# Optimization experiments

Hardware: AMD Instinct MI355X
Metric: run time of the kernel (lower is better)

## Reference

```python
import jax, jax.numpy as jnp
import numpy as np

B, T, C, H = 4, 4096, 1024, 128

def setup_inputs() -> dict:
    key = jax.random.key(0)
    kx, kq, kk, kv = jax.random.split(key, 4)
    s = 1.0 / np.sqrt(C)  # linear-layer-like init scale
    return {
        "x": jax.random.normal(kx, (B, T, C), dtype=jnp.float32),
        "Wq": jax.random.normal(kq, (C, H), dtype=jnp.float32) * s,
        "Wk": jax.random.normal(kk, (C, H), dtype=jnp.float32) * s,
        "Wv": jax.random.normal(kv, (C, H), dtype=jnp.float32) * s,
    }

def reference(x, Wq, Wk, Wv):
    # q,k,v: [B,T,H]
    q = jnp.einsum('btc,ch->bth', x, Wq)
    k = jnp.einsum('btc,ch->bth', x, Wk)
    v = jnp.einsum('btc,ch->bth', x, Wv)
    # scores: [B,T,T]  (NOTE: source applies no 1/sqrt(H) scaling)
    wei = jnp.einsum('bth,bih->bti', q, k)
    t = x.shape[1]
    causal = jnp.tril(jnp.ones((t, t), dtype=bool))
    wei = jnp.where(causal, wei, -jnp.inf)
    probs = jax.nn.softmax(wei, axis=-1)
    out = jnp.einsum('btj,bjh->bth', probs, v)
    return out
```

## Files before the change

### kernel.cpp

```cpp
#include <hip/hip_runtime.h>

#define B_ 4
#define T_ 4096
#define C_ 1024
#define H_ 128

typedef __attribute__((ext_vector_type(8))) __bf16 bf16x8;
typedef __attribute__((ext_vector_type(8))) unsigned short u16x8;
typedef __attribute__((ext_vector_type(4))) float f32x4;
typedef __attribute__((ext_vector_type(4))) unsigned int u32x4;

__device__ __forceinline__ unsigned short f2bf(float f) {
  unsigned int u = __float_as_uint(f);
  return (unsigned short)((u + 0x7FFFu + ((u >> 16) & 1u)) >> 16);
}
__device__ __forceinline__ float bf2f(unsigned short h) {
  return __uint_as_float((unsigned)h << 16);
}
__device__ __forceinline__ bf16x8 ldb8(const unsigned short* p) {
  return *(const bf16x8*)(const void*)p;
}
__device__ __forceinline__ void async16(void* lds, const void* g) {
  __builtin_amdgcn_global_load_lds(
      (const __attribute__((address_space(1))) unsigned int*)g,
      (__attribute__((address_space(3))) unsigned int*)lds, 16, 0, 0);
}
__device__ __forceinline__ void split8a(const float* f, bf16x8& hi, bf16x8& lo) {
  u16x8 h, l;
#pragma unroll
  for (int j = 0; j < 8; j++) {
    h[j] = f2bf(f[j]);
    l[j] = f2bf(f[j] - bf2f(h[j]));
  }
  hi = __builtin_bit_cast(bf16x8, h);
  lo = __builtin_bit_cast(bf16x8, l);
}


__global__ void wt_k(const float* __restrict__ Wq, const float* __restrict__ Wk,
                     const float* __restrict__ Wv, unsigned short* __restrict__ Whi,
                     unsigned short* __restrict__ Wlo) {
  __shared__ float tile[32][33];
  int m = blockIdx.z;
  const float* W = (m == 0) ? Wq : ((m == 1) ? Wk : Wv);
  int c0 = blockIdx.x * 32, h0 = blockIdx.y * 32;
  int tx = threadIdx.x, ty = threadIdx.y;
#pragma unroll
  for (int i = 0; i < 4; i++)
    tile[ty + 8 * i][tx] = W[(size_t)(c0 + ty + 8 * i) * H_ + h0 + tx];
  __syncthreads();
  size_t base = (size_t)m * H_ * C_;
#pragma unroll
  for (int i = 0; i < 4; i++) {
    float f = tile[tx][ty + 8 * i];
    unsigned short hi = f2bf(f);
    int h = h0 + ty + 8 * i;
    int kg = c0 + tx;
    int w0 = kg >> 6, c = (kg >> 3) & 7, e = kg & 7;
    size_t idx = base + (size_t)h * C_ + w0 * 64 + ((c + (h & 7)) & 7) * 8 + e;
    Whi[idx] = hi;
    if (m < 2) Wlo[idx] = f2bf(f - bf2f(hi));
  }
}

__global__ __launch_bounds__(256, 3) void qkv_k(
    const float* __restrict__ x, const unsigned short* __restrict__ Whi,
    const unsigned short* __restrict__ Wlo, unsigned short* __restrict__ Qhi,
    unsigned short* __restrict__ Qlo, unsigned short* __restrict__ Khf,
    unsigned short* __restrict__ Klf, unsigned short* __restrict__ Vf) {
  int m = blockIdx.x % 3;
  int r0 = (blockIdx.x / 3) * 64;
  __shared__ __align__(16) float sx[64 * 64];
  __shared__ __align__(16) unsigned short swh[128 * 64];
  __shared__ __align__(16) unsigned short swl[128 * 64];
  int tid = threadIdx.x;
  int lane = tid & 63, wave = tid >> 6;
  int l15 = lane & 15, quad = lane >> 4;
  const unsigned short* Wmh = Whi + (size_t)m * H_ * C_;
  const unsigned short* Wml = Wlo + (size_t)m * H_ * C_;
  f32x4 acc[8];
#pragma unroll
  for (int n = 0; n < 8; n++) acc[n] = (f32x4){0.f, 0.f, 0.f, 0.f};

  for (int k0 = 0; k0 < C_; k0 += 64) {
    __syncthreads();
#pragma unroll
    for (int i = 0; i < 4; i++) {
      int s = (wave * 4 + i) * 64 + lane;
      {
        int tr = s >> 4, p = s & 15;
        async16((unsigned short*)sx + (size_t)(wave * 4 + i) * 512,
                x + (size_t)(r0 + tr) * C_ + k0 + ((p - tr) & 15) * 4);
      }
      {
        int hr = s >> 3, p = s & 7;
        async16(swh + (size_t)(wave * 4 + i) * 512,
                Wmh + (size_t)hr * C_ + k0 + p * 8);
        if (m < 2)
          async16(swl + (size_t)(wave * 4 + i) * 512,
                  Wml + (size_t)hr * C_ + k0 + p * 8);
      }
    }
    __syncthreads();
#pragma unroll
    for (int kk = 0; kk < 2; kk++) {
      float xa[8];
#pragma unroll
      for (int half = 0; half < 2; half++) {
        int p = (kk * 8 + quad * 2 + half + l15) & 15;
        *(f32x4*)&xa[half * 4] =
            *(const f32x4*)(const void*)(sx + (wave * 16 + l15) * 64 + p * 4);
      }
      bf16x8 ahi, alo;
      split8a(xa, ahi, alo);
      if (m < 2) {
#pragma unroll
        for (int n = 0; n < 8; n++) {
          int p = (kk * 4 + quad + l15) & 7;
          bf16x8 bhi = ldb8(swh + (n * 16 + l15) * 64 + p * 8);
          bf16x8 blo = ldb8(swl + (n * 16 + l15) * 64 + p * 8);
          acc[n] = __builtin_amdgcn_mfma_f32_16x16x32_bf16(ahi, bhi, acc[n], 0, 0, 0);
          acc[n] = __builtin_amdgcn_mfma_f32_16x16x32_bf16(alo, bhi, acc[n], 0, 0, 0);
          acc[n] = __builtin_amdgcn_mfma_f32_16x16x32_bf16(ahi, blo, acc[n], 0, 0, 0);
        }
      } else {
#pragma unroll
        for (int n = 0; n < 8; n++) {
          int p = (kk * 4 + quad + l15) & 7;
          bf16x8 bhi = ldb8(swh + (n * 16 + l15) * 64 + p * 8);
          acc[n] = __builtin_amdgcn_mfma_f32_16x16x32_bf16(ahi, bhi, acc[n], 0, 0, 0);
        }
      }
    }
  }
  int ob = r0 + wave * 16 + quad * 4;
  if (m == 0) {
#pragma unroll
    for (int n8 = 0; n8 < 8; n8++)
#pragma unroll
      for (int r = 0; r < 4; r++) {
        float f = acc[n8][r];
        unsigned short hi = f2bf(f);
        size_t idx = (size_t)(ob + r) * H_ + n8 * 16 + l15;
        Qhi[idx] = hi;
        Qlo[idx] = f2bf(f - bf2f(hi));
      }
  } else if (m == 1) {
#pragma unroll
    for (int n8 = 0; n8 < 8; n8++)
#pragma unroll
      for (int r = 0; r < 4; r++) {
        int gr = ob + r;
        int bb = gr >> 12, t = gr & (T_ - 1);
        int kt = t >> 6, tr = t & 63, nf = tr >> 4, lk = tr & 15;
        int h = n8 * 16 + l15;
        int kkf = h >> 5, qk = (h >> 3) & 3, e = h & 7;
        size_t idx = (size_t)bb * T_ * H_ +
                     (size_t)((kt * 16 + nf * 4 + kkf) * 64 + qk * 16 + lk) * 8 + e;
        float f = acc[n8][r];
        unsigned short hi = f2bf(f);
        Khf[idx] = hi;
        Klf[idx] = f2bf(f - bf2f(hi));
      }
  } else {
#pragma unroll
    for (int n8 = 0; n8 < 8; n8++)
#pragma unroll
      for (int r = 0; r < 4; r++) {
        int gr = ob + r;
        int bb = gr >> 12, t = gr & (T_ - 1);
        int kt = t >> 6, ks = (t >> 5) & 1, qv = (t >> 3) & 3, jj = t & 7;
        size_t idx = (size_t)bb * T_ * H_ +
                     (size_t)((kt * 16 + ks * 8 + n8) * 64 + qv * 16 + l15) * 8 + jj;
        Vf[idx] = f2bf(acc[n8][r]);
      }
  }
}

__device__ __forceinline__ bf16x8 sm_tile(f32x4* s, float& mr, float& lr,
                                          f32x4* o, int lane) {
  int l15 = lane & 15, quad = lane >> 4;
  float mx = fmaxf(fmaxf(fmaxf(s[0][0], s[0][1]), fmaxf(s[0][2], s[0][3])),
                   fmaxf(fmaxf(s[1][0], s[1][1]), fmaxf(s[1][2], s[1][3])));
  mx = fmaxf(mx, __shfl_xor(mx, 16));
  mx = fmaxf(mx, __shfl_xor(mx, 32));
  float mi = fmaxf(mr, mx);
  float al = __expf(mr - mi);
  mr = mi;
#pragma unroll
  for (int n16 = 0; n16 < 2; n16++)
#pragma unroll
    for (int r = 0; r < 4; r++) s[n16][r] = __expf(s[n16][r] - mi);
  float sum = ((s[0][0] + s[0][1]) + (s[0][2] + s[0][3])) +
              ((s[1][0] + s[1][1]) + (s[1][2] + s[1][3]));
  sum += __shfl_xor(sum, 16);
  sum += __shfl_xor(sum, 32);
  lr = lr * al + sum;
  float alo[4];
#pragma unroll
  for (int r = 0; r < 4; r++) alo[r] = __shfl(al, quad * 4 + r);
#pragma unroll
  for (int nv = 0; nv < 8; nv++)
#pragma unroll
    for (int r = 0; r < 4; r++) o[nv][r] *= alo[r];
  unsigned W[2][2];
#pragma unroll
  for (int n16 = 0; n16 < 2; n16++)
#pragma unroll
    for (int j = 0; j < 2; j++)
      W[n16][j] = (unsigned)f2bf(s[n16][2 * j]) |
                  ((unsigned)f2bf(s[n16][2 * j + 1]) << 16);
  int base = ((lane >> 4) & 1) * 32 + l15;
  unsigned A[4];
#pragma unroll
  for (int a = 0; a < 4; a++) {
    int src = base + (a >> 1) * 16;
    unsigned lo = (unsigned)__shfl((int)W[0][a & 1], src);
    unsigned hi = (unsigned)__shfl((int)W[1][a & 1], src);
    A[a] = (lane & 32) ? hi : lo;
  }
  u32x4 aw = (u32x4){A[0], A[1], A[2], A[3]};
  return __builtin_bit_cast(bf16x8, aw);
}

__global__ __launch_bounds__(256, 2) void flash4_k(
    const unsigned short* __restrict__ Qhi, const unsigned short* __restrict__ Qlo,
    const unsigned short* __restrict__ Khf, const unsigned short* __restrict__ Klf,
    const unsigned short* __restrict__ Vf, float* __restrict__ opart,
    float2* __restrict__ mlpart) {
  __shared__ __align__(16) unsigned short skh[2][4096];
  __shared__ __align__(16) unsigned short skl[2][4096];
  __shared__ __align__(16) unsigned short sv[2][4096];
  int tid = threadIdx.x;
  int wave = tid >> 6, lane = tid & 63;
  int l15 = lane & 15, quad = lane >> 4;

  int n = blockIdx.x;
  int h = n >> 4;
  int p = (h < 16) ? (31 - h) : (h - 16);
  int g = n & 15;
  int sp = g >> 2, b = g & 3;
  int q0 = p << 7;
  int ktB = sp * (p + 1);
  int nt = p + 1;
  size_t boff = (size_t)b * T_ * H_;
  const unsigned short* Khb = Khf + boff;
  const unsigned short* Klb = Klf + boff;
  const unsigned short* Vb = Vf + boff;

  bf16x8 qh0[4], ql0[4], qh1[4], ql1[4];
  {
    const unsigned short* qrh =
        Qhi + boff + (size_t)(q0 + wave * 32 + l15) * H_ + quad * 8;
    const unsigned short* qrl =
        Qlo + boff + (size_t)(q0 + wave * 32 + l15) * H_ + quad * 8;
#pragma unroll
    for (int kk = 0; kk < 4; kk++) {
      qh0[kk] = ldb8(qrh + kk * 32);
      ql0[kk] = ldb8(qrl + kk * 32);
      qh1[kk] = ldb8(qrh + 16 * H_ + kk * 32);
      ql1[kk] = ldb8(qrl + 16 * H_ + kk * 32);
    }
  }
  f32x4 o0[8], o1[8];
#pragma unroll
  for (int nn = 0; nn < 8; nn++) {
    o0[nn] = (f32x4){0.f, 0.f, 0.f, 0.f};
    o1[nn] = (f32x4){0.f, 0.f, 0.f, 0.f};
  }
  float mr0 = -1e30f, mr1 = -1e30f, lr0 = 0.f, lr1 = 0.f;

  int rmin = q0 + wave * 32;
  int ch = wave * 2;

#define STAGE(kt32_, d_)                                                        \
  {                                                                             \
    size_t gbase = (size_t)(kt32_)*4096 + (size_t)ch * 512 + (size_t)lane * 8;  \
    async16(&skh[d_][ch * 512], Khb + gbase);                                   \
    async16(&skh[d_][(ch + 1) * 512], Khb + gbase + 512);                       \
    async16(&skl[d_][ch * 512], Klb + gbase);                                   \
    async16(&skl[d_][(ch + 1) * 512], Klb + gbase + 512);                       \
    async16(&sv[d_][ch * 512], Vb + gbase);                                     \
    async16(&sv[d_][(ch + 1) * 512], Vb + gbase + 512);                         \
  }

  STAGE(ktB, 0);
  int cur = 0;
  for (int it = 0; it < nt; ++it) {
    int kt32 = ktB + it;
    if (it + 1 < nt) {
      STAGE(kt32 + 1, cur ^ 1);
      asm volatile("s_waitcnt vmcnt(6)" ::: "memory");
    } else {
      asm volatile("s_waitcnt vmcnt(0)" ::: "memory");
    }
    __builtin_amdgcn_s_barrier();
    int c0k = kt32 << 5;
    bool t1a = (c0k <= rmin + 31);
    bool t0a = (c0k <= rmin + 15);
    if (t1a) {
      f32x4 s0[2], s1[2];
#pragma unroll
      for (int n16 = 0; n16 < 2; ++n16) {
        s0[n16] = (f32x4){0.f, 0.f, 0.f, 0.f};
        s1[n16] = (f32x4){0.f, 0.f, 0.f, 0.f};
      }
      __builtin_amdgcn_s_setprio(1);
#pragma unroll
      for (int n16 = 0; n16 < 2; ++n16) {
        bf16x8 kh[4], kl[4];
#pragma unroll
        for (int kk = 0; kk < 4; kk++) {
          kh[kk] = ldb8(&skh[cur][(n16 * 4 + kk) * 512 + lane * 8]);
          kl[kk] = ldb8(&skl[cur][(n16 * 4 + kk) * 512 + lane * 8]);
        }
#pragma unroll
        for (int kk = 0; kk < 4; kk++) {
          s1[n16] = __builtin_amdgcn_mfma_f32_16x16x32_bf16(kh[kk], qh1[kk], s1[n16], 0, 0, 0);
          s1[n16] = __builtin_amdgcn_mfma_f32_16x16x32_bf16(kh[kk], ql1[kk], s1[n16], 0, 0, 0);
          s1[n16] = __builtin_amdgcn_mfma_f32_16x16x32_bf16(kl[kk], qh1[kk], s1[n16], 0, 0, 0);
          if (t0a) {
            s0[n16] = __builtin_amdgcn_mfma_f32_16x16x32_bf16(kh[kk], qh0[kk], s0[n16], 0, 0, 0);
            s0[n16] = __builtin_amdgcn_mfma_f32_16x16x32_bf16(kh[kk], ql0[kk], s0[n16], 0, 0, 0);
            s0[n16] = __builtin_amdgcn_mfma_f32_16x16x32_bf16(kl[kk], qh0[kk], s0[n16], 0, 0, 0);
          }
        }
      }
      __builtin_amdgcn_s_setprio(0);
      if (c0k + 31 > rmin + 16) {
        int row1 = rmin + 16 + l15;
#pragma unroll
        for (int n16 = 0; n16 < 2; ++n16)
#pragma unroll
          for (int r = 0; r < 4; r++) {
            int col = c0k + n16 * 16 + quad * 4 + r;
            if (col > row1) s1[n16][r] = -1e30f;
          }
      }
      if (t0a && c0k + 31 > rmin) {
        int row0 = rmin + l15;
#pragma unroll
        for (int n16 = 0; n16 < 2; ++n16)
#pragma unroll
          for (int r = 0; r < 4; r++) {
            int col = c0k + n16 * 16 + quad * 4 + r;
            if (col > row0) s0[n16][r] = -1e30f;
          }
      }
      bf16x8 pa1 = sm_tile(s1, mr1, lr1, o1, lane);
      bf16x8 pa0;
      if (t0a) pa0 = sm_tile(s0, mr0, lr0, o0, lane);
      __builtin_amdgcn_s_setprio(1);
#pragma unroll
      for (int nv = 0; nv < 8; ++nv) {
        bf16x8 vf = ldb8(&sv[cur][nv * 512 + lane * 8]);
        o1[nv] = __builtin_amdgcn_mfma_f32_16x16x32_bf16(pa1, vf, o1[nv], 0, 0, 0);
        if (t0a)
          o0[nv] = __builtin_amdgcn_mfma_f32_16x16x32_bf16(pa0, vf, o0[nv], 0, 0, 0);
      }
      __builtin_amdgcn_s_setprio(0);
    }
    __builtin_amdgcn_s_barrier();
    cur ^= 1;
  }
#undef STAGE

  size_t obase = (size_t)((b * 32 + p) * 4 + sp) * (128 * 128);
  size_t mbase = (size_t)((b * 32 + p) * 4 + sp) * 128;
  int wr0 = wave * 32 + quad * 4;
#pragma unroll
  for (int nn = 0; nn < 8; nn++)
#pragma unroll
    for (int r = 0; r < 4; r++) {
      opart[obase + (size_t)(wr0 + r) * 128 + nn * 16 + l15] = o0[nn][r];
      opart[obase + (size_t)(wr0 + 16 + r) * 128 + nn * 16 + l15] = o1[nn][r];
    }
  if (quad == 0) {
    mlpart[mbase + wave * 32 + l15] = make_float2(mr0, lr0);
    mlpart[mbase + wave * 32 + 16 + l15] = make_float2(mr1, lr1);
  }
}

__global__ __launch_bounds__(256) void comb_k(const float* __restrict__ opart,
                                              const float2* __restrict__ mlpart,
                                              float* __restrict__ out) {
  int gid = blockIdx.x * 256 + threadIdx.x;
  int row = gid >> 4;
  int c0 = (gid & 15) << 3;
  int b = row >> 12, t = row & (T_ - 1);
  int p = t >> 7, r = t & 127;
  size_t base = (size_t)(b * 32 + p) * 4;
  float2 ml[4];
#pragma unroll
  for (int s = 0; s < 4; s++) ml[s] = mlpart[base * 128 + s * 128 + r];
  float M = fmaxf(fmaxf(ml[0].x, ml[1].x), fmaxf(ml[2].x, ml[3].x));
  float w[4], L = 0.f;
#pragma unroll
  for (int s = 0; s < 4; s++) {
    w[s] = __expf(ml[s].x - M);
    L += w[s] * ml[s].y;
  }
  float invL = 1.0f / L;
  f32x4 a0 = (f32x4){0.f, 0.f, 0.f, 0.f}, a1 = a0;
#pragma unroll
  for (int s = 0; s < 4; s++) {
    const float* src = opart + (base + s) * (128 * 128) + (size_t)r * 128 + c0;
    a0 += *(const f32x4*)(const void*)src * w[s];
    a1 += *(const f32x4*)(const void*)(src + 4) * w[s];
  }
  float* op = out + ((size_t)b * T_ + t) * H_ + c0;
  *(f32x4*)(void*)op = a0 * invL;
  *(f32x4*)(void*)(op + 4) = a1 * invL;
}

extern "C" void kernel_launch(void* const* d_in, const int* in_sizes, int n_in,
                              void* d_out, int out_size, void* d_ws, size_t ws_size,
                              hipStream_t stream) {
  const float* x  = (const float*)d_in[0];
  const float* Wq = (const float*)d_in[1];
  const float* Wk = (const float*)d_in[2];
  const float* Wv = (const float*)d_in[3];
  const size_t BTH = (size_t)B_ * T_ * H_;
  unsigned short* Whi = (unsigned short*)d_ws;
  unsigned short* Wlo = Whi + 3 * H_ * C_;
  unsigned short* Vf  = Wlo + 2 * H_ * C_;
  unsigned short* Qhi = Vf + BTH;
  unsigned short* Qlo = Qhi + BTH;
  unsigned short* Khf = Qlo + BTH;
  unsigned short* Klf = Khf + BTH;
  float* opart = (float*)(void*)(Klf + BTH);
  float2* mlpart = (float2*)(void*)(opart + 4 * BTH);
  float* out = (float*)d_out;

  wt_k<<<dim3(32, 4, 3), dim3(32, 8), 0, stream>>>(Wq, Wk, Wv, Whi, Wlo);
  qkv_k<<<3 * (B_ * T_ / 64), 256, 0, stream>>>(x, Whi, Wlo, Qhi, Qlo, Khf, Klf, Vf);
  flash4_k<<<512, 256, 0, stream>>>(Qhi, Qlo, Khf, Klf, Vf, opart, mlpart);
  comb_k<<<(B_ * T_ * 16) / 256, 256, 0, stream>>>(opart, mlpart, out);
}
```

Baseline: 221.8 us.

## Triple-buffer async loads in QKV projection and flash attention kernels

The QKV projection kernel moves from a synchronous 64-wide K loop (sync, load, sync, compute) to a 32-wide K step with a three-stage asynchronous LDS pipeline and vmcnt-based waits. The weight swizzle layout changes to match the 32-element rows. The flash attention kernel goes from double to triple buffering of K/V tiles, prefetching two tiles ahead. Both changes aim to hide global load latency behind MFMA work, at the cost of more LDS per block, which may reduce occupancy (qkv launch bounds drop from 3 to 2 blocks).

```diff
diff --git a/kernel.cpp b/kernel.cpp
--- a/kernel.cpp
+++ b/kernel.cpp
@@ -35,6 +35,7 @@
   hi = __builtin_bit_cast(bf16x8, h);
   lo = __builtin_bit_cast(bf16x8, l);
 }
+#define VMC(n) asm volatile("s_waitcnt vmcnt(" #n ")" ::: "memory")
 
 
 __global__ void wt_k(const float* __restrict__ Wq, const float* __restrict__ Wk,
@@ -56,69 +57,92 @@
     unsigned short hi = f2bf(f);
     int h = h0 + ty + 8 * i;
     int kg = c0 + tx;
-    int w0 = kg >> 6, c = (kg >> 3) & 7, e = kg & 7;
-    size_t idx = base + (size_t)h * C_ + w0 * 64 + ((c + (h & 7)) & 7) * 8 + e;
+    int w0 = kg >> 5, c = (kg >> 3) & 3, e = kg & 7;
+    size_t idx = base + (size_t)h * C_ + w0 * 32 + ((c + h) & 3) * 8 + e;
     Whi[idx] = hi;
     if (m < 2) Wlo[idx] = f2bf(f - bf2f(hi));
   }
 }
 
-__global__ __launch_bounds__(256, 3) void qkv_k(
+__device__ __forceinline__ void stage_x(float* dst, const float* xs,
+                                        int wave, int lane) {
+#pragma unroll
+  for (int i = 0; i < 2; i++) {
+    int s = wave * 128 + i * 64 + lane;
+    int tr = s >> 3, px = s & 7;
+    async16(dst + wave * 512 + i * 256,
+            xs + (size_t)tr * C_ + ((px - tr) & 7) * 4);
+  }
+}
+__device__ __forceinline__ void stage_w(unsigned short* dst,
+                                        const unsigned short* Ws,
+                                        int wave, int lane) {
+#pragma unroll
+  for (int i = 0; i < 2; i++) {
+    int s = wave * 128 + i * 64 + lane;
+    int hr = s >> 2, p = s & 3;
+    async16(dst + wave * 1024 + i * 512, Ws + (size_t)hr * C_ + p * 8);
+  }
+}
+
+__global__ __launch_bounds__(256, 2) void qkv_k(
     const float* __restrict__ x, const unsigned short* __restrict__ Whi,
     const unsigned short* __restrict__ Wlo, unsigned short* __restrict__ Qhi,
     unsigned short* __restrict__ Qlo, unsigned short* __restrict__ Khf,
     unsigned short* __restrict__ Klf, unsigned short* __restrict__ Vf) {
+  __shared__ __align__(16) float sx[3][64 * 32];
+  __shared__ __align__(16) unsigned short swh[3][128 * 32];
+  __shared__ __align__(16) unsigned short swl[3][128 * 32];
   int m = blockIdx.x % 3;
   int r0 = (blockIdx.x / 3) * 64;
-  __shared__ __align__(16) float sx[64 * 64];
-  __shared__ __align__(16) unsigned short swh[128 * 64];
-  __shared__ __align__(16) unsigned short swl[128 * 64];
   int tid = threadIdx.x;
   int lane = tid & 63, wave = tid >> 6;
   int l15 = lane & 15, quad = lane >> 4;
+  const float* xb = x + (size_t)r0 * C_;
   const unsigned short* Wmh = Whi + (size_t)m * H_ * C_;
   const unsigned short* Wml = Wlo + (size_t)m * H_ * C_;
   f32x4 acc[8];
 #pragma unroll
   for (int n = 0; n < 8; n++) acc[n] = (f32x4){0.f, 0.f, 0.f, 0.f};
 
-  for (int k0 = 0; k0 < C_; k0 += 64) {
-    __syncthreads();
-#pragma unroll
-    for (int i = 0; i < 4; i++) {
-      int s = (wave * 4 + i) * 64 + lane;
-      {
-        int tr = s >> 4, p = s & 15;
-        async16((unsigned short*)sx + (size_t)(wave * 4 + i) * 512,
-                x + (size_t)(r0 + tr) * C_ + k0 + ((p - tr) & 15) * 4);
-      }
-      {
-        int hr = s >> 3, p = s & 7;
-        async16(swh + (size_t)(wave * 4 + i) * 512,
-                Wmh + (size_t)hr * C_ + k0 + p * 8);
-        if (m < 2)
-          async16(swl + (size_t)(wave * 4 + i) * 512,
-                  Wml + (size_t)hr * C_ + k0 + p * 8);
-      }
-    }
-    __syncthreads();
-#pragma unroll
-    for (int kk = 0; kk < 2; kk++) {
+#define QSTG(t_, d_)                         \
+  {                                          \
+    stage_x(sx[d_], xb + (t_)*32, wave, lane);             \
+    stage_w(swh[d_], Wmh + (t_)*32, wave, lane);           \
+    if (m < 2) stage_w(swl[d_], Wml + (t_)*32, wave, lane); \
+  }
+
+  QSTG(0, 0);
+  QSTG(1, 1);
+  int cur = 0;
+  const int NT = C_ / 32;
+  for (int it = 0; it < NT; ++it) {
+    int st = cur + 2;
+    if (st >= 3) st -= 3;
+    if (it + 2 < NT) {
+      QSTG(it + 2, st);
+      if (m < 2) VMC(12); else VMC(8);
+    } else if (it + 1 < NT) {
+      if (m < 2) VMC(6); else VMC(4);
+    } else {
+      VMC(0);
+    }
+    __builtin_amdgcn_s_barrier();
+    {
       float xa[8];
-#pragma unroll
-      for (int half = 0; half < 2; half++) {
-        int p = (kk * 8 + quad * 2 + half + l15) & 15;
-        *(f32x4*)&xa[half * 4] =
-            *(const f32x4*)(const void*)(sx + (wave * 16 + l15) * 64 + p * 4);
-      }
+      const float* xrow = &sx[cur][(wave * 16 + l15) * 32];
+      *(f32x4*)&xa[0] =
+          *(const f32x4*)(const void*)(xrow + ((quad * 2 + l15) & 7) * 4);
+      *(f32x4*)&xa[4] =
+          *(const f32x4*)(const void*)(xrow + ((quad * 2 + 1 + l15) & 7) * 4);
       bf16x8 ahi, alo;
       split8a(xa, ahi, alo);
+      int slw = ((quad + l15) & 3) * 8;
       if (m < 2) {
 #pragma unroll
         for (int n = 0; n < 8; n++) {
-          int p = (kk * 4 + quad + l15) & 7;
-          bf16x8 bhi = ldb8(swh + (n * 16 + l15) * 64 + p * 8);
-          bf16x8 blo = ldb8(swl + (n * 16 + l15) * 64 + p * 8);
+          bf16x8 bhi = ldb8(&swh[cur][(n * 16 + l15) * 32 + slw]);
+          bf16x8 blo = ldb8(&swl[cur][(n * 16 + l15) * 32 + slw]);
           acc[n] = __builtin_amdgcn_mfma_f32_16x16x32_bf16(ahi, bhi, acc[n], 0, 0, 0);
           acc[n] = __builtin_amdgcn_mfma_f32_16x16x32_bf16(alo, bhi, acc[n], 0, 0, 0);
           acc[n] = __builtin_amdgcn_mfma_f32_16x16x32_bf16(ahi, blo, acc[n], 0, 0, 0);
@@ -126,13 +150,16 @@
       } else {
 #pragma unroll
         for (int n = 0; n < 8; n++) {
-          int p = (kk * 4 + quad + l15) & 7;
-          bf16x8 bhi = ldb8(swh + (n * 16 + l15) * 64 + p * 8);
+          bf16x8 bhi = ldb8(&swh[cur][(n * 16 + l15) * 32 + slw]);
           acc[n] = __builtin_amdgcn_mfma_f32_16x16x32_bf16(ahi, bhi, acc[n], 0, 0, 0);
         }
       }
     }
-  }
+    __builtin_amdgcn_s_barrier();
+    cur = (cur == 2) ? 0 : cur + 1;
+  }
+#undef QSTG
+
   int ob = r0 + wave * 16 + quad * 4;
   if (m == 0) {
 #pragma unroll
@@ -223,14 +250,14 @@
   return __builtin_bit_cast(bf16x8, aw);
 }
 
-__global__ __launch_bounds__(256, 2) void flash4_k(
+__global__ __launch_bounds__(256, 2) void flash5_k(
     const unsigned short* __restrict__ Qhi, const unsigned short* __restrict__ Qlo,
     const unsigned short* __restrict__ Khf, const unsigned short* __restrict__ Klf,
     const unsigned short* __restrict__ Vf, float* __restrict__ opart,
     float2* __restrict__ mlpart) {
-  __shared__ __align__(16) unsigned short skh[2][4096];
-  __shared__ __align__(16) unsigned short skl[2][4096];
-  __shared__ __align__(16) unsigned short sv[2][4096];
+  __shared__ __align__(16) unsigned short skh[3][4096];
+  __shared__ __align__(16) unsigned short skl[3][4096];
+  __shared__ __align__(16) unsigned short sv[3][4096];
   int tid = threadIdx.x;
   int wave = tid >> 6, lane = tid & 63;
   int l15 = lane & 15, quad = lane >> 4;
@@ -285,14 +312,19 @@
   }
 
   STAGE(ktB, 0);
+  if (nt > 1) STAGE(ktB + 1, 1);
   int cur = 0;
   for (int it = 0; it < nt; ++it) {
     int kt32 = ktB + it;
-    if (it + 1 < nt) {
-      STAGE(kt32 + 1, cur ^ 1);
-      asm volatile("s_waitcnt vmcnt(6)" ::: "memory");
+    int st = cur + 2;
+    if (st >= 3) st -= 3;
+    if (it + 2 < nt) {
+      STAGE(kt32 + 2, st);
+      VMC(12);
+    } else if (it + 1 < nt) {
+      VMC(6);
     } else {
-      asm volatile("s_waitcnt vmcnt(0)" ::: "memory");
+      VMC(0);
     }
     __builtin_amdgcn_s_barrier();
     int c0k = kt32 << 5;
@@ -361,7 +393,7 @@
       __builtin_amdgcn_s_setprio(0);
     }
     __builtin_amdgcn_s_barrier();
-    cur ^= 1;
+    cur = (cur == 2) ? 0 : cur + 1;
   }
 #undef STAGE
 
@@ -434,6 +466,6 @@
 
   wt_k<<<dim3(32, 4, 3), dim3(32, 8), 0, stream>>>(Wq, Wk, Wv, Whi, Wlo);
   qkv_k<<<3 * (B_ * T_ / 64), 256, 0, stream>>>(x, Whi, Wlo, Qhi, Qlo, Khf, Klf, Vf);
-  flash4_k<<<512, 256, 0, stream>>>(Qhi, Qlo, Khf, Klf, Vf, opart, mlpart);
+  flash5_k<<<512, 256, 0, stream>>>(Qhi, Qlo, Khf, Klf, Vf, opart, mlpart);
   comb_k<<<(B_ * T_ * 16) / 256, 256, 0, stream>>>(opart, mlpart, out);
 }
```

Measured after the change: 252.6 us. +13.9%, slower.

## Split attention KV range into eight balanced chunks per query block

Applied to the files above, without the earlier changes.

Increases the split-K factor of the flash attention kernel from 4 to 8, dividing the 32-key tiles evenly across splits with a remainder distribution, and launches 1024 blocks instead of 512. The block ordering interleaves long and short query blocks so the work is better balanced. The combine kernel now merges 8 partial results per row. The extra partial outputs double the opart workspace and the combine traffic, and some splits may have no tiles to process.

```diff
diff --git a/kernel.cpp b/kernel.cpp
--- a/kernel.cpp
+++ b/kernel.cpp
@@ -35,6 +35,7 @@
   hi = __builtin_bit_cast(bf16x8, h);
   lo = __builtin_bit_cast(bf16x8, l);
 }
+#define VMC(n) asm volatile("s_waitcnt vmcnt(" #n ")" ::: "memory")
 
 
 __global__ void wt_k(const float* __restrict__ Wq, const float* __restrict__ Wk,
@@ -223,7 +224,7 @@
   return __builtin_bit_cast(bf16x8, aw);
 }
 
-__global__ __launch_bounds__(256, 2) void flash4_k(
+__global__ __launch_bounds__(256, 2) void flash6_k(
     const unsigned short* __restrict__ Qhi, const unsigned short* __restrict__ Qlo,
     const unsigned short* __restrict__ Khf, const unsigned short* __restrict__ Klf,
     const unsigned short* __restrict__ Vf, float* __restrict__ opart,
@@ -236,13 +237,14 @@
   int l15 = lane & 15, quad = lane >> 4;
 
   int n = blockIdx.x;
-  int h = n >> 4;
-  int p = (h < 16) ? (31 - h) : (h - 16);
-  int g = n & 15;
+  int k = n >> 8, h = (n >> 5) & 7, g = n & 31;
+  int p = (k == 0) ? (31 - h) : ((k == 1) ? (16 + h) : ((k == 2) ? (15 - h) : h));
   int sp = g >> 2, b = g & 3;
   int q0 = p << 7;
-  int ktB = sp * (p + 1);
-  int nt = p + 1;
+  int NC = 4 * (p + 1);
+  int qq = NC >> 3, rr = NC & 7;
+  int ktB = sp * qq + (sp < rr ? sp : rr);
+  int nt = qq + (sp < rr ? 1 : 0);
   size_t boff = (size_t)b * T_ * H_;
   const unsigned short* Khb = Khf + boff;
   const unsigned short* Klb = Klf + boff;
@@ -284,89 +286,92 @@
     async16(&sv[d_][(ch + 1) * 512], Vb + gbase + 512);                         \
   }
 
-  STAGE(ktB, 0);
-  int cur = 0;
-  for (int it = 0; it < nt; ++it) {
-    int kt32 = ktB + it;
-    if (it + 1 < nt) {
-      STAGE(kt32 + 1, cur ^ 1);
-      asm volatile("s_waitcnt vmcnt(6)" ::: "memory");
-    } else {
-      asm volatile("s_waitcnt vmcnt(0)" ::: "memory");
+  if (nt > 0) {
+    STAGE(ktB, 0);
+    int cur = 0;
+    for (int it = 0; it < nt; ++it) {
+      int kt32 = ktB + it;
+      if (it + 1 < nt) {
+        STAGE(kt32 + 1, cur ^ 1);
+        VMC(6);
+      } else {
+        VMC(0);
+      }
+      __builtin_amdgcn_s_barrier();
+      int c0k = kt32 << 5;
+      bool t1a = (c0k <= rmin + 31);
+      bool t0a = (c0k <= rmin + 15);
+      if (t1a) {
+        f32x4 s0[2], s1[2];
+#pragma unroll
+        for (int n16 = 0; n16 < 2; ++n16) {
+          s0[n16] = (f32x4){0.f, 0.f, 0.f, 0.f};
+          s1[n16] = (f32x4){0.f, 0.f, 0.f, 0.f};
+        }
+        __builtin_amdgcn_s_setprio(1);
+#pragma unroll
+        for (int n16 = 0; n16 < 2; ++n16) {
+          bf16x8 kh[4], kl[4];
+#pragma unroll
+          for (int kk = 0; kk < 4; kk++) {
+            kh[kk] = ldb8(&skh[cur][(n16 * 4 + kk) * 512 + lane * 8]);
+            kl[kk] = ldb8(&skl[cur][(n16 * 4 + kk) * 512 + lane * 8]);
+          }
+#pragma unroll
+          for (int kk = 0; kk < 4; kk++) {
+            s1[n16] = __builtin_amdgcn_mfma_f32_16x16x32_bf16(kh[kk], qh1[kk], s1[n16], 0, 0, 0);
+            s1[n16] = __builtin_amdgcn_mfma_f32_16x16x32_bf16(kh[kk], ql1[kk], s1[n16], 0, 0, 0);
+            s1[n16] = __builtin_amdgcn_mfma_f32_16x16x32_bf16(kl[kk], qh1[kk], s1[n16], 0, 0, 0);
+            if (t0a) {
+              s0[n16] = __builtin_amdgcn_mfma_f32_16x16x32_bf16(kh[kk], qh0[kk], s0[n16], 0, 0, 0);
+              s0[n16] = __builtin_amdgcn_mfma_f32_16x16x32_bf16(kh[kk], ql0[kk], s0[n16], 0, 0, 0);
+              s0[n16] = __builtin_amdgcn_mfma_f32_16x16x32_bf16(kl[kk], qh0[kk], s0[n16], 0, 0, 0);
+            }
+          }
+        }
+        __builtin_amdgcn_s_setprio(0);
+        if (c0k + 31 > rmin + 16) {
+          int row1 = rmin + 16 + l15;
+#pragma unroll
+          for (int n16 = 0; n16 < 2; ++n16)
+#pragma unroll
+            for (int r = 0; r < 4; r++) {
+              int col = c0k + n16 * 16 + quad * 4 + r;
+              if (col > row1) s1[n16][r] = -1e30f;
+            }
+        }
+        if (t0a && c0k + 31 > rmin) {
+          int row0 = rmin + l15;
+#pragma unroll
+          for (int n16 = 0; n16 < 2; ++n16)
+#pragma unroll
+            for (int r = 0; r < 4; r++) {
+              int col = c0k + n16 * 16 + quad * 4 + r;
+              if (col > row0) s0[n16][r] = -1e30f;
+            }
+        }
+        bf16x8 pa1 = sm_tile(s1, mr1, lr1, o1, lane);
+        bf16x8 pa0;
+        if (t0a) pa0 = sm_tile(s0, mr0, lr0, o0, lane);
+        __builtin_amdgcn_s_setprio(1);
+#pragma unroll
+        for (int nv = 0; nv < 8; ++nv) {
+          bf16x8 vf = ldb8(&sv[cur][nv * 512 + lane * 8]);
+          o1[nv] = __builtin_amdgcn_mfma_f32_16x16x32_bf16(pa1, vf, o1[nv], 0, 0, 0);
+          if (t0a)
+            o0[nv] = __builtin_amdgcn_mfma_f32_16x16x32_bf16(pa0, vf, o0[nv], 0, 0, 0);
+        }
+        __builtin_amdgcn_s_setprio(0);
+      }
+      __builtin_amdgcn_s_barrier();
+      cur ^= 1;
     }
-    __builtin_amdgcn_s_barrier();
-    int c0k = kt32 << 5;
-    bool t1a = (c0k <= rmin + 31);
-    bool t0a = (c0k <= rmin + 15);
-    if (t1a) {
-      f32x4 s0[2], s1[2];
-#pragma unroll
-      for (int n16 = 0; n16 < 2; ++n16) {
-        s0[n16] = (f32x4){0.f, 0.f, 0.f, 0.f};
-        s1[n16] = (f32x4){0.f, 0.f, 0.f, 0.f};
-      }
-      __builtin_amdgcn_s_setprio(1);
-#pragma unroll
-      for (int n16 = 0; n16 < 2; ++n16) {
-        bf16x8 kh[4], kl[4];
-#pragma unroll
-        for (int kk = 0; kk < 4; kk++) {
-          kh[kk] = ldb8(&skh[cur][(n16 * 4 + kk) * 512 + lane * 8]);
-          kl[kk] = ldb8(&skl[cur][(n16 * 4 + kk) * 512 + lane * 8]);
-        }
-#pragma unroll
-        for (int kk = 0; kk < 4; kk++) {
-          s1[n16] = __builtin_amdgcn_mfma_f32_16x16x32_bf16(kh[kk], qh1[kk], s1[n16], 0, 0, 0);
-          s1[n16] = __builtin_amdgcn_mfma_f32_16x16x32_bf16(kh[kk], ql1[kk], s1[n16], 0, 0, 0);
-          s1[n16] = __builtin_amdgcn_mfma_f32_16x16x32_bf16(kl[kk], qh1[kk], s1[n16], 0, 0, 0);
-          if (t0a) {
-            s0[n16] = __builtin_amdgcn_mfma_f32_16x16x32_bf16(kh[kk], qh0[kk], s0[n16], 0, 0, 0);
-            s0[n16] = __builtin_amdgcn_mfma_f32_16x16x32_bf16(kh[kk], ql0[kk], s0[n16], 0, 0, 0);
-            s0[n16] = __builtin_amdgcn_mfma_f32_16x16x32_bf16(kl[kk], qh0[kk], s0[n16], 0, 0, 0);
-          }
-        }
-      }
-      __builtin_amdgcn_s_setprio(0);
-      if (c0k + 31 > rmin + 16) {
-        int row1 = rmin + 16 + l15;
-#pragma unroll
-        for (int n16 = 0; n16 < 2; ++n16)
-#pragma unroll
-          for (int r = 0; r < 4; r++) {
-            int col = c0k + n16 * 16 + quad * 4 + r;
-            if (col > row1) s1[n16][r] = -1e30f;
-          }
-      }
-      if (t0a && c0k + 31 > rmin) {
-        int row0 = rmin + l15;
-#pragma unroll
-        for (int n16 = 0; n16 < 2; ++n16)
-#pragma unroll
-          for (int r = 0; r < 4; r++) {
-            int col = c0k + n16 * 16 + quad * 4 + r;
-            if (col > row0) s0[n16][r] = -1e30f;
-          }
-      }
-      bf16x8 pa1 = sm_tile(s1, mr1, lr1, o1, lane);
-      bf16x8 pa0;
-      if (t0a) pa0 = sm_tile(s0, mr0, lr0, o0, lane);
-      __builtin_amdgcn_s_setprio(1);
-#pragma unroll
-      for (int nv = 0; nv < 8; ++nv) {
-        bf16x8 vf = ldb8(&sv[cur][nv * 512 + lane * 8]);
-        o1[nv] = __builtin_amdgcn_mfma_f32_16x16x32_bf16(pa1, vf, o1[nv], 0, 0, 0);
-        if (t0a)
-          o0[nv] = __builtin_amdgcn_mfma_f32_16x16x32_bf16(pa0, vf, o0[nv], 0, 0, 0);
-      }
-      __builtin_amdgcn_s_setprio(0);
-    }
-    __builtin_amdgcn_s_barrier();
-    cur ^= 1;
   }
 #undef STAGE
 
-  size_t obase = (size_t)((b * 32 + p) * 4 + sp) * (128 * 128);
-  size_t mbase = (size_t)((b * 32 + p) * 4 + sp) * 128;
+  size_t slot = (size_t)((b * 32 + p) * 8 + sp);
+  size_t obase = slot * (128 * 128);
+  size_t mbase = slot * 128;
   int wr0 = wave * 32 + quad * 4;
 #pragma unroll
   for (int nn = 0; nn < 8; nn++)
@@ -389,21 +394,23 @@
   int c0 = (gid & 15) << 3;
   int b = row >> 12, t = row & (T_ - 1);
   int p = t >> 7, r = t & 127;
-  size_t base = (size_t)(b * 32 + p) * 4;
-  float2 ml[4];
-#pragma unroll
-  for (int s = 0; s < 4; s++) ml[s] = mlpart[base * 128 + s * 128 + r];
-  float M = fmaxf(fmaxf(ml[0].x, ml[1].x), fmaxf(ml[2].x, ml[3].x));
-  float w[4], L = 0.f;
-#pragma unroll
-  for (int s = 0; s < 4; s++) {
+  size_t base = (size_t)(b * 32 + p) * 8;
+  float2 ml[8];
+#pragma unroll
+  for (int s = 0; s < 8; s++) ml[s] = mlpart[(base + s) * 128 + r];
+  float M = ml[0].x;
+#pragma unroll
+  for (int s = 1; s < 8; s++) M = fmaxf(M, ml[s].x);
+  float w[8], L = 0.f;
+#pragma unroll
+  for (int s = 0; s < 8; s++) {
     w[s] = __expf(ml[s].x - M);
     L += w[s] * ml[s].y;
   }
   float invL = 1.0f / L;
   f32x4 a0 = (f32x4){0.f, 0.f, 0.f, 0.f}, a1 = a0;
 #pragma unroll
-  for (int s = 0; s < 4; s++) {
+  for (int s = 0; s < 8; s++) {
     const float* src = opart + (base + s) * (128 * 128) + (size_t)r * 128 + c0;
     a0 += *(const f32x4*)(const void*)src * w[s];
     a1 += *(const f32x4*)(const void*)(src + 4) * w[s];
@@ -429,11 +436,11 @@
   unsigned short* Khf = Qlo + BTH;
   unsigned short* Klf = Khf + BTH;
   float* opart = (float*)(void*)(Klf + BTH);
-  float2* mlpart = (float2*)(void*)(opart + 4 * BTH);
+  float2* mlpart = (float2*)(void*)(opart + 8 * BTH);
   float* out = (float*)d_out;
 
   wt_k<<<dim3(32, 4, 3), dim3(32, 8), 0, stream>>>(Wq, Wk, Wv, Whi, Wlo);
   qkv_k<<<3 * (B_ * T_ / 64), 256, 0, stream>>>(x, Whi, Wlo, Qhi, Qlo, Khf, Klf, Vf);
-  flash4_k<<<512, 256, 0, stream>>>(Qhi, Qlo, Khf, Klf, Vf, opart, mlpart);
+  flash6_k<<<1024, 256, 0, stream>>>(Qhi, Qlo, Khf, Klf, Vf, opart, mlpart);
   comb_k<<<(B_ * T_ * 16) / 256, 256, 0, stream>>>(opart, mlpart, out);
 }
```

Result: faster. 211.1 us (median of 2 runs) (-4.8%).
